# Kernel tuning notes

Hardware: AMD Instinct MI355X
Metric: run time of the kernel (lower is better)

Reference implementation:

```python
import jax, jax.numpy as jnp
import numpy as np

MARGIN = 0.5
HIERARCHY_LEVEL = 0
EPS = 1e-05


def setup_inputs() -> dict:
    key = jax.random.key(0)
    k1, k2, k3, k4 = jax.random.split(key, 4)
    n, m, d, L, n_classes = 4096, 32768, 128, 2, 100
    embeddings = jax.random.normal(k1, (n, d), dtype=jnp.float32)
    ref_embeddings = jax.random.normal(k2, (m, d), dtype=jnp.float32)
    labels = jax.random.randint(k3, (n, L), 0, n_classes, dtype=jnp.int64)
    ref_labels = jax.random.randint(k4, (m, L), 0, n_classes, dtype=jnp.int64)
    return {"embeddings": embeddings, "labels": labels,
            "ref_embeddings": ref_embeddings, "ref_labels": ref_labels}


def reference(embeddings, labels, ref_embeddings, ref_labels):
    # select hierarchy level
    lab = labels[:, HIERARCHY_LEVEL]          # [n]
    ref_lab = ref_labels[:, HIERARCHY_LEVEL]  # [m]
    n = embeddings.shape[0]
    sim = embeddings @ ref_embeddings.T       # [n, m]
    same = lab[:, None] == ref_lab[None, :]   # [n, m] bool
    # positive pairs: same label and sim < 1 - eps -> contribute (1 - sim)
    pos_mask = same & (sim < 1.0 - EPS)
    # negative pairs: different label and sim > margin -> contribute sim
    neg_mask = (~same) & (sim > MARGIN)
    pos_loss = jnp.sum(jnp.where(pos_mask, 1.0 - sim, 0.0))
    neg_loss = jnp.sum(jnp.where(neg_mask, sim, 0.0))
    return (pos_loss + neg_loss) / n
```

## Files before the change

kernel.cpp:

```cpp
#include <hip/hip_runtime.h>
#include <stdint.h>

#define N_EMB 4096
#define M_REF 32768
#define D_K   128
#define BM    128
#define BN    128
#define NCOLTILES 16
#define COLCHUNK (BN * NCOLTILES)
#define NCCHUNK (M_REF / COLCHUNK)
#define NROWT  (N_EMB / BM)

typedef __attribute__((ext_vector_type(8))) short short8;
typedef __attribute__((ext_vector_type(4))) float float4v;

static __device__ __forceinline__ unsigned short f2bf(float f) {
    unsigned int u = __builtin_bit_cast(unsigned int, f);
    u += 0x7FFFu + ((u >> 16) & 1u);
    return (unsigned short)(u >> 16);
}

__global__ void cvt_kernel(const float* __restrict__ emb, const float* __restrict__ ref,
                           unsigned short* __restrict__ aw, unsigned short* __restrict__ bw) {
    const int NA4 = N_EMB * D_K / 4;
    const int NB4 = M_REF * D_K / 4;
    int stride = gridDim.x * blockDim.x;
    for (int i = blockIdx.x * blockDim.x + threadIdx.x; i < NA4 + NB4; i += stride) {
        const float4* src;
        unsigned short* dst;
        int j;
        if (i < NA4) { src = (const float4*)emb; dst = aw; j = i; }
        else         { src = (const float4*)ref; dst = bw; j = i - NA4; }
        float4 v = src[j];
        ushort4 o;
        o.x = f2bf(v.x); o.y = f2bf(v.y); o.z = f2bf(v.z); o.w = f2bf(v.w);
        *(ushort4*)(dst + (size_t)j * 4) = o;
    }
}

static __device__ __forceinline__ void gld_lds16(const void* g, void* l) {
    __builtin_amdgcn_global_load_lds((__attribute__((address_space(1))) void*)g,
                                     (__attribute__((address_space(3))) void*)l,
                                     16, 0, 0);
}

__launch_bounds__(256, 2)
__global__ void xbm_kernel(const unsigned short* __restrict__ aw,
                           const unsigned short* __restrict__ bw,
                           const int* __restrict__ lab,
                           const int* __restrict__ rlab,
                           float* __restrict__ out) {
    __shared__ unsigned short a_sm[BM * D_K];
    __shared__ unsigned short b_sm[BN * D_K];
    __shared__ float red_sm[4];

    const int tid  = threadIdx.x;
    const int lane = tid & 63;
    const int wave = tid >> 6;
    const int wm = wave >> 1, wn = wave & 1;
    const int quad = lane >> 4;
    const int l15  = lane & 15;

    const int rtile  = blockIdx.x >> 4;
    const int cchunk = blockIdx.x & 15;
    const int row0 = rtile * BM;
    const int col0 = cchunk * COLCHUNK;

    #pragma unroll
    for (int i = 0; i < 8; ++i) {
        int c  = i * 256 + tid;
        int r  = c >> 4;
        int ch = c & 15;
        int sc = ch ^ (r & 15);
        gld_lds16((const char*)aw + ((size_t)(row0 + r) * D_K + sc * 8) * 2,
                  (char*)a_sm + (size_t)c * 16);
    }

    int labv[4][4];
    #pragma unroll
    for (int mt = 0; mt < 4; ++mt)
        #pragma unroll
        for (int r = 0; r < 4; ++r) {
            int row = row0 + wm * 64 + mt * 16 + quad * 4 + r;
            labv[mt][r] = lab[row * 2];
        }

    __syncthreads();

    short8 a_reg[4][4];
    #pragma unroll
    for (int mt = 0; mt < 4; ++mt) {
        int ml = wm * 64 + mt * 16 + l15;
        #pragma unroll
        for (int ks = 0; ks < 4; ++ks) {
            int ch = ks * 4 + quad;
            int cs = ch ^ (ml & 15);
            a_reg[mt][ks] = *(const short8*)(a_sm + (size_t)ml * D_K + cs * 8);
        }
    }

    float loss = 0.0f;

    for (int t = 0; t < NCOLTILES; ++t) {
        const int cbase = col0 + t * BN;

        #pragma unroll
        for (int i = 0; i < 8; ++i) {
            int c  = i * 256 + tid;
            int r  = c >> 4;
            int ch = c & 15;
            int sc = ch ^ (r & 15);
            gld_lds16((const char*)bw + ((size_t)(cbase + r) * D_K + sc * 8) * 2,
                      (char*)b_sm + (size_t)c * 16);
        }
        __syncthreads();

        float4v acc[4][4] = {};
        #pragma unroll
        for (int ks = 0; ks < 4; ++ks) {
            short8 b_reg[4];
            #pragma unroll
            for (int nt = 0; nt < 4; ++nt) {
                int nl = wn * 64 + nt * 16 + l15;
                int ch = ks * 4 + quad;
                int cs = ch ^ (nl & 15);
                b_reg[nt] = *(const short8*)(b_sm + (size_t)nl * D_K + cs * 8);
            }
            #pragma unroll
            for (int mt = 0; mt < 4; ++mt)
                #pragma unroll
                for (int nt = 0; nt < 4; ++nt)
                    acc[mt][nt] = __builtin_amdgcn_mfma_f32_16x16x32_bf16(
                        a_reg[mt][ks], b_reg[nt], acc[mt][nt], 0, 0, 0);
        }
        __syncthreads();

        int rl[4];
        #pragma unroll
        for (int nt = 0; nt < 4; ++nt) {
            int cix = cbase + wn * 64 + nt * 16 + l15;
            rl[nt] = rlab[cix * 2];
        }
        #pragma unroll
        for (int mt = 0; mt < 4; ++mt)
            #pragma unroll
            for (int nt = 0; nt < 4; ++nt)
                #pragma unroll
                for (int r = 0; r < 4; ++r) {
                    float s = acc[mt][nt][r];
                    float pos = fmaxf(1.0f - s, 0.0f);
                    float neg = (s > 0.5f) ? s : 0.0f;
                    loss += (labv[mt][r] == rl[nt]) ? pos : neg;
                }
    }

    #pragma unroll
    for (int off = 32; off > 0; off >>= 1)
        loss += __shfl_down(loss, off, 64);
    if (lane == 0) red_sm[wave] = loss;
    __syncthreads();
    if (tid == 0) {
        float v = (red_sm[0] + red_sm[1] + red_sm[2] + red_sm[3]) * (1.0f / (float)N_EMB);
        atomicAdd(out, v);
    }
}

extern "C" void kernel_launch(void* const* d_in, const int* in_sizes, int n_in,
                              void* d_out, int out_size, void* d_ws, size_t ws_size,
                              hipStream_t stream) {
    const float* emb     = (const float*)d_in[0];
    const int*   labels  = (const int*)d_in[1];
    const float* ref     = (const float*)d_in[2];
    const int*   rlabels = (const int*)d_in[3];
    float* out = (float*)d_out;

    unsigned short* aw = (unsigned short*)d_ws;
    unsigned short* bw = aw + (size_t)N_EMB * D_K;

    hipMemsetAsync(d_out, 0, sizeof(float), stream);
    cvt_kernel<<<512, 256, 0, stream>>>(emb, ref, aw, bw);
    xbm_kernel<<<NROWT * NCCHUNK, 256, 0, stream>>>(aw, bw, labels, rlabels, out);
}
```

Baseline: 118.0 us.

## Double-buffer B tiles, stage ref labels in LDS, fold output zeroing into convert kernel

Splits LDS into two B-tile buffers so the async global-to-LDS load of the next column tile overlaps the MFMA work on the current one. The A tile reuses the first buffer at startup. Reference labels for the whole column chunk are copied into LDS once instead of being read from global memory every tile. It also removes the separate memset launch by zeroing the output inside the convert kernel, unrolls that kernel over a fixed 768-block grid, and keeps four partial sums. LDS use grows, which may affect occupancy at two blocks per CU.

```diff
diff --git a/kernel.cpp b/kernel.cpp
--- a/kernel.cpp
+++ b/kernel.cpp
@@ -20,12 +20,17 @@
     return (unsigned short)(u >> 16);
 }
 
+#define CVT_THREADS (768 * 256)
+
 __global__ void cvt_kernel(const float* __restrict__ emb, const float* __restrict__ ref,
-                           unsigned short* __restrict__ aw, unsigned short* __restrict__ bw) {
+                           unsigned short* __restrict__ aw, unsigned short* __restrict__ bw,
+                           float* __restrict__ out) {
     const int NA4 = N_EMB * D_K / 4;
-    const int NB4 = M_REF * D_K / 4;
-    int stride = gridDim.x * blockDim.x;
-    for (int i = blockIdx.x * blockDim.x + threadIdx.x; i < NA4 + NB4; i += stride) {
+    int i0 = blockIdx.x * blockDim.x + threadIdx.x;
+    if (i0 == 0) *out = 0.0f;
+    #pragma unroll
+    for (int k = 0; k < 6; ++k) {
+        int i = i0 + k * CVT_THREADS;
         const float4* src;
         unsigned short* dst;
         int j;
@@ -43,6 +48,71 @@
                                      (__attribute__((address_space(3))) void*)l,
                                      16, 0, 0);
 }
+static __device__ __forceinline__ void gld_lds4(const void* g, void* l) {
+    __builtin_amdgcn_global_load_lds((__attribute__((address_space(1))) void*)g,
+                                     (__attribute__((address_space(3))) void*)l,
+                                     4, 0, 0);
+}
+
+static __device__ __forceinline__ void stage_tile(const unsigned short* __restrict__ g,
+                                                  unsigned short* lbuf, int tid) {
+    const int rbase = tid >> 4;
+    const int ch    = tid & 15;
+    const int sc    = ch ^ rbase;
+    const char* g0 = (const char*)g + ((size_t)rbase * D_K + sc * 8) * 2;
+    char* l0 = (char*)lbuf + (size_t)tid * 16;
+    #pragma unroll
+    for (int i = 0; i < 8; ++i)
+        gld_lds16(g0 + (size_t)i * (16 * D_K * 2), l0 + i * 4096);
+}
+
+static __device__ __forceinline__ void stage_labels(const int* __restrict__ rlab,
+                                                    int col0, int* lsm, int tid) {
+    const char* g0 = (const char*)rlab + ((size_t)col0 * 2 + (size_t)tid * 2) * 4;
+    char* l0 = (char*)lsm + (size_t)tid * 4;
+    #pragma unroll
+    for (int i = 0; i < 8; ++i)
+        gld_lds4(g0 + (size_t)i * 2048, l0 + i * 1024);
+}
+
+static __device__ __forceinline__ void compute_tile(
+    const unsigned short* __restrict__ bp,
+    const short8 a_reg[4][4], const int b_off[16],
+    const int labv[4][4], const int* __restrict__ rl_t,
+    int wn, int l15, float lsum[4])
+{
+    float4v acc[4][4] = {};
+    #pragma unroll
+    for (int ks = 0; ks < 4; ++ks) {
+        short8 b_reg[4];
+        #pragma unroll
+        for (int nt = 0; nt < 4; ++nt)
+            b_reg[nt] = *(const short8*)((const char*)bp + b_off[ks * 4 + nt]);
+        #pragma unroll
+        for (int mt = 0; mt < 4; ++mt)
+            #pragma unroll
+            for (int nt = 0; nt < 4; ++nt)
+                acc[mt][nt] = __builtin_amdgcn_mfma_f32_16x16x32_bf16(
+                    a_reg[mt][ks], b_reg[nt], acc[mt][nt], 0, 0, 0);
+    }
+
+    int rl[4];
+    #pragma unroll
+    for (int nt = 0; nt < 4; ++nt)
+        rl[nt] = rl_t[wn * 64 + nt * 16 + l15];
+
+    #pragma unroll
+    for (int mt = 0; mt < 4; ++mt)
+        #pragma unroll
+        for (int nt = 0; nt < 4; ++nt)
+            #pragma unroll
+            for (int r = 0; r < 4; ++r) {
+                float s = acc[mt][nt][r];
+                float pos = fmaxf(1.0f - s, 0.0f);
+                float neg = (s > 0.5f) ? s : 0.0f;
+                lsum[r] += (labv[mt][r] == rl[nt]) ? pos : neg;
+            }
+}
 
 __launch_bounds__(256, 2)
 __global__ void xbm_kernel(const unsigned short* __restrict__ aw,
@@ -50,8 +120,8 @@
                            const int* __restrict__ lab,
                            const int* __restrict__ rlab,
                            float* __restrict__ out) {
-    __shared__ unsigned short a_sm[BM * D_K];
-    __shared__ unsigned short b_sm[BN * D_K];
+    __shared__ unsigned short b_sm[2][BN * D_K];
+    __shared__ int rl_sm[COLCHUNK];
     __shared__ float red_sm[4];
 
     const int tid  = threadIdx.x;
@@ -66,24 +136,16 @@
     const int row0 = rtile * BM;
     const int col0 = cchunk * COLCHUNK;
 
-    #pragma unroll
-    for (int i = 0; i < 8; ++i) {
-        int c  = i * 256 + tid;
-        int r  = c >> 4;
-        int ch = c & 15;
-        int sc = ch ^ (r & 15);
-        gld_lds16((const char*)aw + ((size_t)(row0 + r) * D_K + sc * 8) * 2,
-                  (char*)a_sm + (size_t)c * 16);
-    }
+    stage_tile(aw + (size_t)row0 * D_K, b_sm[0], tid);
+    stage_tile(bw + (size_t)col0 * D_K, b_sm[1], tid);
+    stage_labels(rlab, col0, rl_sm, tid);
 
     int labv[4][4];
     #pragma unroll
     for (int mt = 0; mt < 4; ++mt)
         #pragma unroll
-        for (int r = 0; r < 4; ++r) {
-            int row = row0 + wm * 64 + mt * 16 + quad * 4 + r;
-            labv[mt][r] = lab[row * 2];
-        }
+        for (int r = 0; r < 4; ++r)
+            labv[mt][r] = lab[(row0 + wm * 64 + mt * 16 + quad * 4 + r) * 2];
 
     __syncthreads();
 
@@ -93,67 +155,38 @@
         int ml = wm * 64 + mt * 16 + l15;
         #pragma unroll
         for (int ks = 0; ks < 4; ++ks) {
-            int ch = ks * 4 + quad;
-            int cs = ch ^ (ml & 15);
-            a_reg[mt][ks] = *(const short8*)(a_sm + (size_t)ml * D_K + cs * 8);
+            int cs = (ks * 4 + quad) ^ l15;
+            a_reg[mt][ks] = *(const short8*)(b_sm[0] + (size_t)ml * D_K + cs * 8);
         }
     }
 
-    float loss = 0.0f;
-
-    for (int t = 0; t < NCOLTILES; ++t) {
-        const int cbase = col0 + t * BN;
-
-        #pragma unroll
-        for (int i = 0; i < 8; ++i) {
-            int c  = i * 256 + tid;
-            int r  = c >> 4;
-            int ch = c & 15;
-            int sc = ch ^ (r & 15);
-            gld_lds16((const char*)bw + ((size_t)(cbase + r) * D_K + sc * 8) * 2,
-                      (char*)b_sm + (size_t)c * 16);
+    int b_off[16];
+    #pragma unroll
+    for (int ks = 0; ks < 4; ++ks)
+        #pragma unroll
+        for (int nt = 0; nt < 4; ++nt) {
+            int nl = wn * 64 + nt * 16 + l15;
+            int cs = (ks * 4 + quad) ^ l15;
+            b_off[ks * 4 + nt] = (nl * D_K + cs * 8) * 2;
         }
+
+    float lsum[4] = {0.0f, 0.0f, 0.0f, 0.0f};
+
+    __syncthreads();
+
+    #pragma unroll 1
+    for (int t = 0; t < NCOLTILES; t += 2) {
+        stage_tile(bw + (size_t)(col0 + (t + 1) * BN) * D_K, b_sm[0], tid);
+        compute_tile(b_sm[1], a_reg, b_off, labv, rl_sm + t * BN, wn, l15, lsum);
         __syncthreads();
 
-        float4v acc[4][4] = {};
-        #pragma unroll
-        for (int ks = 0; ks < 4; ++ks) {
-            short8 b_reg[4];
-            #pragma unroll
-            for (int nt = 0; nt < 4; ++nt) {
-                int nl = wn * 64 + nt * 16 + l15;
-                int ch = ks * 4 + quad;
-                int cs = ch ^ (nl & 15);
-                b_reg[nt] = *(const short8*)(b_sm + (size_t)nl * D_K + cs * 8);
-            }
-            #pragma unroll
-            for (int mt = 0; mt < 4; ++mt)
-                #pragma unroll
-                for (int nt = 0; nt < 4; ++nt)
-                    acc[mt][nt] = __builtin_amdgcn_mfma_f32_16x16x32_bf16(
-                        a_reg[mt][ks], b_reg[nt], acc[mt][nt], 0, 0, 0);
-        }
+        if (t + 2 < NCOLTILES)
+            stage_tile(bw + (size_t)(col0 + (t + 2) * BN) * D_K, b_sm[1], tid);
+        compute_tile(b_sm[0], a_reg, b_off, labv, rl_sm + (t + 1) * BN, wn, l15, lsum);
         __syncthreads();
-
-        int rl[4];
-        #pragma unroll
-        for (int nt = 0; nt < 4; ++nt) {
-            int cix = cbase + wn * 64 + nt * 16 + l15;
-            rl[nt] = rlab[cix * 2];
-        }
-        #pragma unroll
-        for (int mt = 0; mt < 4; ++mt)
-            #pragma unroll
-            for (int nt = 0; nt < 4; ++nt)
-                #pragma unroll
-                for (int r = 0; r < 4; ++r) {
-                    float s = acc[mt][nt][r];
-                    float pos = fmaxf(1.0f - s, 0.0f);
-                    float neg = (s > 0.5f) ? s : 0.0f;
-                    loss += (labv[mt][r] == rl[nt]) ? pos : neg;
-                }
-    }
-
+    }
+
+    float loss = (lsum[0] + lsum[1]) + (lsum[2] + lsum[3]);
     #pragma unroll
     for (int off = 32; off > 0; off >>= 1)
         loss += __shfl_down(loss, off, 64);
@@ -177,7 +210,6 @@
     unsigned short* aw = (unsigned short*)d_ws;
     unsigned short* bw = aw + (size_t)N_EMB * D_K;
 
-    hipMemsetAsync(d_out, 0, sizeof(float), stream);
-    cvt_kernel<<<512, 256, 0, stream>>>(emb, ref, aw, bw);
+    cvt_kernel<<<768, 256, 0, stream>>>(emb, ref, aw, bw, out);
     xbm_kernel<<<NROWT * NCCHUNK, 256, 0, stream>>>(aw, bw, labels, rlabels, out);
 }
```

Result: no change. 118.7 us (+0.6%).
